# Kernel tuning notes

Hardware: AMD Instinct MI355X
Metric: run time of the kernel (lower is better)

The kernel has to match this reference:

```python
import jax, jax.numpy as jnp
import numpy as np
from jax import lax

KEEP_RATIO = 0.5
GROUP_RATIO = 0.5
TOPK = 2


def setup_inputs() -> dict:
    key = jax.random.key(0)
    k1, k2, k3 = jax.random.split(key, 3)
    x = jax.random.normal(k1, (64, 577, 768), dtype=jnp.float32)
    cls_attn = jax.random.uniform(k2, (64, 576), dtype=jnp.float32)
    expert_distribution = jax.random.uniform(k3, (64, 577, 16), dtype=jnp.float32)
    return {"x": x, "cls_attn": cls_attn, "expert_distribution": expert_distribution}


def _build_graph(spa, B, S, k):
    """Cosine kNN graph per batch + to_undirected dedup + iterative directional
    degree filter (KthAverageAggregator.directional_filter). Returns fixed-size
    candidate edge arrays (src, dst) with a validity mask."""
    Nn = B * S
    # cosine similarity kNN (pyg knn_graph cosine=True, loop=False)
    cn = spa / jnp.clip(jnp.linalg.norm(spa, axis=-1, keepdims=True), 1e-12)
    sim = jnp.einsum('bse,bte->bst', cn, cn)                    # [B,S,S]
    sim = jnp.where(jnp.eye(S, dtype=bool)[None], -2.0, sim)    # exclude self
    _, nbr = lax.top_k(sim, k)                                  # [B,S,k] neighbors j of node i
    offs = (jnp.arange(B) * S)[:, None, None]
    src = (nbr + offs).reshape(-1)                              # flow source_to_target: edge (j -> i)
    dst = jnp.broadcast_to(jnp.arange(S)[None, :, None] + offs, (B, S, k)).reshape(-1)
    # to_undirected with coalesce (dedup) -> fixed-size candidates + unique mask
    cs = jnp.concatenate([src, dst])
    cd = jnp.concatenate([dst, src])
    keyv = cs * Nn + cd
    perm = jnp.argsort(keyv)
    es, ed, ks = cs[perm], cd[perm], keyv[perm]
    uniq = jnp.concatenate([jnp.array([True]), ks[1:] != ks[:-1]])

    def deg_in(m):
        return jax.ops.segment_sum(m.astype(jnp.int32), ed, num_segments=Nn)

    # directional filter: keep edge (u->v) iff in_degree[v] > in_degree[u]; iterate to fixpoint
    d0 = deg_in(uniq)
    cur0 = uniq & (d0[ed] > d0[es])

    def cond(st):
        return st[0].sum() != st[1]

    def body(st):
        cur, _ = st
        d = deg_in(cur)
        return (cur & (d[ed] > d[es]), cur.sum())

    valid, _ = lax.while_loop(cond, body, (cur0, jnp.int32(-1)))
    return es, ed, valid


def reference(x, cls_attn, expert_distribution):
    B, Np1, D = x.shape
    N = Np1 - 1
    cls_tk = x[:, :1]                     # [B,1,D]
    patch_x = x[:, 1:]                    # [B,N,D]
    ped = expert_distribution[:, 1:]      # [B,N,E]
    # cls_attn_reordering: sort patches by cls attention, descending
    order = jnp.argsort(-cls_attn, axis=1)
    ca = jnp.take_along_axis(cls_attn, order, axis=1)
    px = jnp.take_along_axis(patch_x, order[:, :, None], axis=1)
    ped = jnp.take_along_axis(ped, order[:, :, None], axis=1)
    density = int(N * KEEP_RATIO)
    S = N - density
    patch_tk, skip = px[:, :density], px[:, density:]
    nsca, sca = ca[:, :density], ca[:, density:]
    spa = ped[:, density:]                # skip tokens' expert distributions (kNN criteria)
    Nn = B * S

    es, ed, valid = _build_graph(spa, B, S, TOPK)

    # propagate (sum aggregation) with self loops
    xs = skip.reshape(Nn, D)
    w = valid.astype(xs.dtype)[:, None]
    avg = jax.ops.segment_sum(xs[es] * w, ed, num_segments=Nn) + xs
    avg = avg.reshape(B, S, D)

    # node degree over edges[0] (sources), self loops add 1
    deg_src = jax.ops.segment_sum(valid.astype(jnp.int32), es, num_segments=Nn) + 1
    nd = deg_src.reshape(B, S)
    G = int(S * GROUP_RATIO)
    _, gidx = lax.top_k(nd, G)            # [B,G]

    summ = jnp.take_along_axis(avg, gidx[:, :, None], axis=1)
    sca_sel = jnp.take_along_axis(sca, gidx, axis=1)
    tokens = jnp.concatenate([cls_tk, patch_tk, summ], axis=1)
    attn = jnp.concatenate([nsca, sca_sel], axis=-1)
    return tokens, attn
```

## Files before the change

### kernel.cpp

```cpp
#include <hip/hip_runtime.h>
#include <hip/hip_bf16.h>
#include <math.h>

#define BB   64
#define NP1  577
#define DD   768
#define NNP  576
#define DENS 288
#define SS   288
#define KNN  2
#define EPB  (SS*KNN*2)
#define GG   144
#define TOK  (1+DENS+GG)
#define ATT  (DENS+GG)

__global__ __launch_bounds__(256) void k_sort(const float* __restrict__ ca,
                                              int* __restrict__ order,
                                              float* __restrict__ ca_sorted) {
    __shared__ float v[1024];
    __shared__ int   ix[1024];
    const int b = blockIdx.x;
    for (int i = threadIdx.x; i < 1024; i += 256) {
        if (i < NNP) { v[i] = ca[b*NNP + i]; }
        else         { v[i] = -INFINITY; }
        ix[i] = i;
    }
    __syncthreads();
    for (int k = 2; k <= 1024; k <<= 1) {
        for (int j = k >> 1; j > 0; j >>= 1) {
            for (int t = threadIdx.x; t < 1024; t += 256) {
                int p = t ^ j;
                if (p > t) {
                    float va = v[t], vb = v[p];
                    int   ia = ix[t], ib = ix[p];
                    bool lpt = (vb > va) || (vb == va && ib < ia);
                    bool up  = ((t & k) == 0);
                    if (lpt == up) { v[t] = vb; v[p] = va; ix[t] = ib; ix[p] = ia; }
                }
            }
            __syncthreads();
        }
    }
    for (int i = threadIdx.x; i < NNP; i += 256) {
        order[b*NNP + i]     = ix[i];
        ca_sorted[b*NNP + i] = v[i];
    }
}

__global__ __launch_bounds__(320) void k_graph(const float* __restrict__ ex,
                                               const int* __restrict__ order,
                                               const float* __restrict__ ca_sorted,
                                               unsigned* __restrict__ rowptr,
                                               unsigned* __restrict__ col,
                                               int* __restrict__ selnode,
                                               int* __restrict__ selrow,
                                               float* __restrict__ out_attn) {
    __shared__ float    cn[SS][16];
    __shared__ int      nbrs[SS][2];
    __shared__ unsigned edge[EPB];
    __shared__ unsigned char act[EPB];
    __shared__ unsigned deg[SS];
    __shared__ int      ndv[SS];
    __shared__ unsigned scan[320];
    __shared__ int      srow[SS];
    __shared__ int      gsel[GG];
    __shared__ unsigned tot;
    const int b = blockIdx.x, t = threadIdx.x;

    if (t < SS) {
        int src = order[b*NNP + DENS + t];
        srow[t] = b*NP1 + 1 + src;
        const float* row = ex + ((size_t)b*NP1 + 1 + src) * 16;
        float vv[16]; float ssum = 0.f;
        #pragma unroll
        for (int e = 0; e < 16; e++) { vv[e] = row[e]; ssum += vv[e]*vv[e]; }
        float inv = 1.0f / fmaxf(sqrtf(ssum), 1e-12f);
        #pragma unroll
        for (int e = 0; e < 16; e++) cn[t][e] = vv[e]*inv;
    }
    __syncthreads();

    if (t < SS) {
        float my[16];
        #pragma unroll
        for (int e = 0; e < 16; e++) my[e] = cn[t][e];
        float v1 = -3.f, v2 = -3.f; int i1 = -1, i2 = -1;
        for (int j = 0; j < SS; j++) {
            if (j == t) continue;
            float s = 0.f;
            #pragma unroll
            for (int e = 0; e < 16; e++) s = fmaf(my[e], cn[j][e], s);
            if (s > v1)      { v2 = v1; i2 = i1; v1 = s; i1 = j; }
            else if (s > v2) { v2 = s;  i2 = j; }
        }
        nbrs[t][0] = i1; nbrs[t][1] = i2;
    }
    if (t == 0) tot = 0;
    __syncthreads();

    if (t < SS) {
        #pragma unroll
        for (int j = 0; j < 2; j++) {
            int p = nbrs[t][j];
            bool mutual = (nbrs[p][0] == t) || (nbrs[p][1] == t);
            unsigned char pv = (!mutual || (t < p)) ? 1 : 0;
            int q = (t*2 + j) * 2;
            edge[q]   = ((unsigned)p << 16) | (unsigned)t;
            edge[q+1] = ((unsigned)t << 16) | (unsigned)p;
            act[q] = pv; act[q+1] = pv;
        }
    }
    __syncthreads();

    int prev = -1;
    while (true) {
        if (t < SS) deg[t] = 0;
        __syncthreads();
        for (int e = t; e < EPB; e += 320)
            if (act[e]) atomicAdd(&deg[edge[e] & 0xFFFFu], 1u);
        __syncthreads();
        unsigned cnt = 0;
        for (int e = t; e < EPB; e += 320) {
            if (act[e]) {
                unsigned ed = edge[e];
                if (!(deg[ed & 0xFFFFu] > deg[ed >> 16])) act[e] = 0;
                cnt += act[e];
            }
        }
        for (int o = 32; o > 0; o >>= 1) cnt += __shfl_down(cnt, o, 64);
        if ((t & 63) == 0 && cnt) atomicAdd(&tot, cnt);
        __syncthreads();
        int total = (int)tot;
        __syncthreads();
        if (t == 0) tot = 0;
        if (total == prev) break;
        prev = total;
    }

    if (t < SS) deg[t] = 0;
    __syncthreads();
    for (int e = t; e < EPB; e += 320)
        if (act[e]) atomicAdd(&deg[edge[e] >> 16], 1u);
    __syncthreads();
    if (t < SS) ndv[t] = (int)deg[t] + 1;
    __syncthreads();

    if (t < SS) {
        int mine = ndv[t], rank = 0;
        for (int m = 0; m < SS; m++) {
            int v = ndv[m];
            rank += (v > mine) || (v == mine && m < t);
        }
        if (rank < GG) gsel[rank] = t;
    }
    if (t < SS) deg[t] = 0;
    __syncthreads();

    if (t < GG) {
        int n = gsel[t];
        selnode[b*GG + t] = n;
        selrow[b*GG + t]  = srow[n];
        out_attn[b*ATT + DENS + t] = ca_sorted[b*NNP + DENS + n];
    }
    if (t < DENS) out_attn[b*ATT + t] = ca_sorted[b*NNP + t];

    for (int e = t; e < EPB; e += 320)
        if (act[e]) atomicAdd(&deg[edge[e] & 0xFFFFu], 1u);
    __syncthreads();

    unsigned dv = (t < SS) ? deg[t] : 0;
    scan[t] = dv;
    __syncthreads();
    for (int off = 1; off < SS; off <<= 1) {
        unsigned add = (t >= off) ? scan[t - off] : 0u;
        __syncthreads();
        scan[t] += add;
        __syncthreads();
    }
    if (t < SS) {
        rowptr[b*(SS+1) + t + 1] = scan[t];
        deg[t] = scan[t] - dv;
    }
    if (t == 0) rowptr[b*(SS+1)] = 0;
    __syncthreads();

    for (int e = t; e < EPB; e += 320) {
        if (act[e]) {
            unsigned ed = edge[e];
            unsigned pos = atomicAdd(&deg[ed & 0xFFFFu], 1u);
            col[b*EPB + pos] = (unsigned)srow[ed >> 16];
        }
    }
}

__global__ __launch_bounds__(256) void k_tokens(const float* __restrict__ x,
                                                const int* __restrict__ order,
                                                const int* __restrict__ selnode,
                                                const int* __restrict__ selrow,
                                                const unsigned* __restrict__ rowptr,
                                                const unsigned* __restrict__ col,
                                                float* __restrict__ out) {
    const int wid  = threadIdx.x >> 6;
    const int lane = threadIdx.x & 63;
    int row = blockIdx.x*4 + wid;
    if (row >= BB*TOK) return;
    int b  = row / TOK;
    int tk = row - b*TOK;
    float4* __restrict__ orow = (float4*)(out + (size_t)row*DD);

    if (tk <= DENS) {
        int srcrow = (tk == 0) ? (b*NP1) : (b*NP1 + 1 + order[b*NNP + (tk-1)]);
        const float4* s4 = (const float4*)(x + (size_t)srcrow*DD);
        #pragma unroll
        for (int q = 0; q < 3; q++) orow[lane + q*64] = s4[lane + q*64];
    } else {
        int r = tk - 1 - DENS;
        int n = selnode[b*GG + r];
        int g = b*(SS+1) + n;
        unsigned e0 = rowptr[g], e1 = rowptr[g+1];
        float4 acc0 = make_float4(0,0,0,0), acc1 = acc0, acc2 = acc0;
        for (unsigned e = e0; e < e1; e++) {
            const float4* s4 = (const float4*)(x + (size_t)col[b*EPB + e]*DD);
            float4 a = s4[lane], bq = s4[lane + 64], c = s4[lane + 128];
            acc0.x += a.x;  acc0.y += a.y;  acc0.z += a.z;  acc0.w += a.w;
            acc1.x += bq.x; acc1.y += bq.y; acc1.z += bq.z; acc1.w += bq.w;
            acc2.x += c.x;  acc2.y += c.y;  acc2.z += c.z;  acc2.w += c.w;
        }
        const float4* s4 = (const float4*)(x + (size_t)selrow[b*GG + r]*DD);
        float4 a = s4[lane], bq = s4[lane + 64], c = s4[lane + 128];
        acc0.x += a.x;  acc0.y += a.y;  acc0.z += a.z;  acc0.w += a.w;
        acc1.x += bq.x; acc1.y += bq.y; acc1.z += bq.z; acc1.w += bq.w;
        acc2.x += c.x;  acc2.y += c.y;  acc2.z += c.z;  acc2.w += c.w;
        orow[lane]       = acc0;
        orow[lane + 64]  = acc1;
        orow[lane + 128] = acc2;
    }
}

extern "C" void kernel_launch(void* const* d_in, const int* in_sizes, int n_in,
                              void* d_out, int out_size, void* d_ws, size_t ws_size,
                              hipStream_t stream) {
    const float* x  = (const float*)d_in[0];
    const float* ca = (const float*)d_in[1];
    const float* ex = (const float*)d_in[2];
    float* out = (float*)d_out;

    char* w = (char*)d_ws;
    int*      order     = (int*)w;      w += (size_t)BB*NNP*4;
    float*    ca_sorted = (float*)w;    w += (size_t)BB*NNP*4;
    unsigned* rowptr    = (unsigned*)w; w += (size_t)BB*(SS+1)*4;
    unsigned* col       = (unsigned*)w; w += (size_t)BB*EPB*4;
    int*      selnode   = (int*)w;      w += (size_t)BB*GG*4;
    int*      selrow    = (int*)w;      w += (size_t)BB*GG*4;

    float* out_attn = out + (size_t)BB*TOK*DD;

    k_sort<<<BB, 256, 0, stream>>>(ca, order, ca_sorted);
    k_graph<<<BB, 320, 0, stream>>>(ex, order, ca_sorted,
                                    rowptr, col, selnode, selrow, out_attn);
    k_tokens<<<(BB*TOK + 3)/4, 256, 0, stream>>>(x, order, selnode, selrow,
                                                 rowptr, col, out);
}
```

Before: 292.3 us.

## Fuse sort into graph kernel using rank-based sort and cheaper fixpoint check

Removes the separate bitonic sort kernel and computes each patch's sorted position by rank counting inside the graph kernel, which now runs 576 threads per batch. The sorted attention values stay in shared memory, so the global ca_sorted round trip goes away. The fixpoint loop now uses a shared changed flag instead of a wave reduction plus atomic edge count. The final in-degree is reused from the loop rather than recomputed, and the cosine matrix is padded to 17 columns to avoid LDS bank conflicts. In exchange, the O(N^2) rank loop adds per-thread work, and the whole graph stage still runs on only 64 blocks.

```diff
diff --git a/kernel.cpp b/kernel.cpp
--- a/kernel.cpp
+++ b/kernel.cpp
@@ -13,67 +13,56 @@
 #define GG   144
 #define TOK  (1+DENS+GG)
 #define ATT  (DENS+GG)
-
-__global__ __launch_bounds__(256) void k_sort(const float* __restrict__ ca,
-                                              int* __restrict__ order,
-                                              float* __restrict__ ca_sorted) {
-    __shared__ float v[1024];
-    __shared__ int   ix[1024];
-    const int b = blockIdx.x;
-    for (int i = threadIdx.x; i < 1024; i += 256) {
-        if (i < NNP) { v[i] = ca[b*NNP + i]; }
-        else         { v[i] = -INFINITY; }
-        ix[i] = i;
-    }
-    __syncthreads();
-    for (int k = 2; k <= 1024; k <<= 1) {
-        for (int j = k >> 1; j > 0; j >>= 1) {
-            for (int t = threadIdx.x; t < 1024; t += 256) {
-                int p = t ^ j;
-                if (p > t) {
-                    float va = v[t], vb = v[p];
-                    int   ia = ix[t], ib = ix[p];
-                    bool lpt = (vb > va) || (vb == va && ib < ia);
-                    bool up  = ((t & k) == 0);
-                    if (lpt == up) { v[t] = vb; v[p] = va; ix[t] = ib; ix[p] = ia; }
-                }
-            }
-            __syncthreads();
-        }
-    }
-    for (int i = threadIdx.x; i < NNP; i += 256) {
-        order[b*NNP + i]     = ix[i];
-        ca_sorted[b*NNP + i] = v[i];
-    }
-}
-
-__global__ __launch_bounds__(320) void k_graph(const float* __restrict__ ex,
-                                               const int* __restrict__ order,
-                                               const float* __restrict__ ca_sorted,
+#define TPB  576
+
+__global__ __launch_bounds__(TPB) void k_graph(const float* __restrict__ ca,
+                                               const float* __restrict__ ex,
+                                               int* __restrict__ order_g,
                                                unsigned* __restrict__ rowptr,
                                                unsigned* __restrict__ col,
                                                int* __restrict__ selnode,
                                                int* __restrict__ selrow,
                                                float* __restrict__ out_attn) {
-    __shared__ float    cn[SS][16];
-    __shared__ int      nbrs[SS][2];
+    __shared__ float    val[NNP];
+    __shared__ float    sortedv[NNP];
+    __shared__ short    sorder[NNP];
+    __shared__ float    cn[SS][17];
+    __shared__ short    nbrs[SS][2];
     __shared__ unsigned edge[EPB];
     __shared__ unsigned char act[EPB];
     __shared__ unsigned deg[SS];
+    __shared__ unsigned indeg[SS];
     __shared__ int      ndv[SS];
-    __shared__ unsigned scan[320];
+    __shared__ unsigned scan[NNP];
     __shared__ int      srow[SS];
-    __shared__ int      gsel[GG];
-    __shared__ unsigned tot;
+    __shared__ short    gsel[GG];
+    __shared__ int      changed;
     const int b = blockIdx.x, t = threadIdx.x;
 
-    if (t < SS) {
-        int src = order[b*NNP + DENS + t];
-        srow[t] = b*NP1 + 1 + src;
-        const float* row = ex + ((size_t)b*NP1 + 1 + src) * 16;
+    float v = ca[b*NNP + t];
+    val[t] = v;
+    __syncthreads();
+    int rank = 0;
+    #pragma unroll 8
+    for (int m = 0; m < NNP; m++) {
+        float u = val[m];
+        rank += (u > v) || (u == v && m < t);
+    }
+    sortedv[rank] = v;
+    sorder[rank]  = (short)t;
+    if (rank < DENS) order_g[b*NNP + rank] = t;
+    __syncthreads();
+
+    if (t < DENS) out_attn[b*ATT + t] = sortedv[t];
+
+    if (t < SS) {
+        int src = sorder[DENS + t];
+        int row = b*NP1 + 1 + src;
+        srow[t] = row;
+        const float* rp = ex + (size_t)row * 16;
         float vv[16]; float ssum = 0.f;
         #pragma unroll
-        for (int e = 0; e < 16; e++) { vv[e] = row[e]; ssum += vv[e]*vv[e]; }
+        for (int e = 0; e < 16; e++) { vv[e] = rp[e]; ssum += vv[e]*vv[e]; }
         float inv = 1.0f / fmaxf(sqrtf(ssum), 1e-12f);
         #pragma unroll
         for (int e = 0; e < 16; e++) cn[t][e] = vv[e]*inv;
@@ -93,9 +82,8 @@
             if (s > v1)      { v2 = v1; i2 = i1; v1 = s; i1 = j; }
             else if (s > v2) { v2 = s;  i2 = j; }
         }
-        nbrs[t][0] = i1; nbrs[t][1] = i2;
-    }
-    if (t == 0) tot = 0;
+        nbrs[t][0] = (short)i1; nbrs[t][1] = (short)i2;
+    }
     __syncthreads();
 
     if (t < SS) {
@@ -112,63 +100,56 @@
     }
     __syncthreads();
 
-    int prev = -1;
     while (true) {
         if (t < SS) deg[t] = 0;
-        __syncthreads();
-        for (int e = t; e < EPB; e += 320)
+        if (t == 0) changed = 0;
+        __syncthreads();
+        #pragma unroll
+        for (int e = t; e < EPB; e += TPB)
             if (act[e]) atomicAdd(&deg[edge[e] & 0xFFFFu], 1u);
         __syncthreads();
-        unsigned cnt = 0;
-        for (int e = t; e < EPB; e += 320) {
+        #pragma unroll
+        for (int e = t; e < EPB; e += TPB) {
             if (act[e]) {
                 unsigned ed = edge[e];
-                if (!(deg[ed & 0xFFFFu] > deg[ed >> 16])) act[e] = 0;
-                cnt += act[e];
+                if (!(deg[ed & 0xFFFFu] > deg[ed >> 16])) { act[e] = 0; changed = 1; }
             }
         }
-        for (int o = 32; o > 0; o >>= 1) cnt += __shfl_down(cnt, o, 64);
-        if ((t & 63) == 0 && cnt) atomicAdd(&tot, cnt);
-        __syncthreads();
-        int total = (int)tot;
-        __syncthreads();
-        if (t == 0) tot = 0;
-        if (total == prev) break;
-        prev = total;
-    }
+        __syncthreads();
+        int ch = changed;
+        __syncthreads();
+        if (!ch) break;
+    }
+    if (t < SS) indeg[t] = deg[t];
+    __syncthreads();
 
     if (t < SS) deg[t] = 0;
     __syncthreads();
-    for (int e = t; e < EPB; e += 320)
+    #pragma unroll
+    for (int e = t; e < EPB; e += TPB)
         if (act[e]) atomicAdd(&deg[edge[e] >> 16], 1u);
     __syncthreads();
     if (t < SS) ndv[t] = (int)deg[t] + 1;
     __syncthreads();
 
     if (t < SS) {
-        int mine = ndv[t], rank = 0;
+        int mine = ndv[t], r = 0;
         for (int m = 0; m < SS; m++) {
-            int v = ndv[m];
-            rank += (v > mine) || (v == mine && m < t);
-        }
-        if (rank < GG) gsel[rank] = t;
-    }
-    if (t < SS) deg[t] = 0;
+            int u = ndv[m];
+            r += (u > mine) || (u == mine && m < t);
+        }
+        if (r < GG) gsel[r] = (short)t;
+    }
     __syncthreads();
 
     if (t < GG) {
         int n = gsel[t];
         selnode[b*GG + t] = n;
         selrow[b*GG + t]  = srow[n];
-        out_attn[b*ATT + DENS + t] = ca_sorted[b*NNP + DENS + n];
-    }
-    if (t < DENS) out_attn[b*ATT + t] = ca_sorted[b*NNP + t];
-
-    for (int e = t; e < EPB; e += 320)
-        if (act[e]) atomicAdd(&deg[edge[e] & 0xFFFFu], 1u);
-    __syncthreads();
-
-    unsigned dv = (t < SS) ? deg[t] : 0;
+        out_attn[b*ATT + DENS + t] = sortedv[DENS + n];
+    }
+
+    unsigned dv = (t < SS) ? indeg[t] : 0u;
     scan[t] = dv;
     __syncthreads();
     for (int off = 1; off < SS; off <<= 1) {
@@ -184,7 +165,8 @@
     if (t == 0) rowptr[b*(SS+1)] = 0;
     __syncthreads();
 
-    for (int e = t; e < EPB; e += 320) {
+    #pragma unroll
+    for (int e = t; e < EPB; e += TPB) {
         if (act[e]) {
             unsigned ed = edge[e];
             unsigned pos = atomicAdd(&deg[ed & 0xFFFFu], 1u);
@@ -246,18 +228,16 @@
     float* out = (float*)d_out;
 
     char* w = (char*)d_ws;
-    int*      order     = (int*)w;      w += (size_t)BB*NNP*4;
-    float*    ca_sorted = (float*)w;    w += (size_t)BB*NNP*4;
-    unsigned* rowptr    = (unsigned*)w; w += (size_t)BB*(SS+1)*4;
-    unsigned* col       = (unsigned*)w; w += (size_t)BB*EPB*4;
-    int*      selnode   = (int*)w;      w += (size_t)BB*GG*4;
-    int*      selrow    = (int*)w;      w += (size_t)BB*GG*4;
+    int*      order   = (int*)w;      w += (size_t)BB*NNP*4;
+    unsigned* rowptr  = (unsigned*)w; w += (size_t)BB*(SS+1)*4;
+    unsigned* col     = (unsigned*)w; w += (size_t)BB*EPB*4;
+    int*      selnode = (int*)w;      w += (size_t)BB*GG*4;
+    int*      selrow  = (int*)w;      w += (size_t)BB*GG*4;
 
     float* out_attn = out + (size_t)BB*TOK*DD;
 
-    k_sort<<<BB, 256, 0, stream>>>(ca, order, ca_sorted);
-    k_graph<<<BB, 320, 0, stream>>>(ex, order, ca_sorted,
-                                    rowptr, col, selnode, selrow, out_attn);
+    k_graph<<<BB, TPB, 0, stream>>>(ca, ex, order, rowptr, col,
+                                    selnode, selrow, out_attn);
     k_tokens<<<(BB*TOK + 3)/4, 256, 0, stream>>>(x, order, selnode, selrow,
                                                  rowptr, col, out);
 }
```

Measured after the change: 282.2 us. 3.5% less time.
